# Kernel optimization log

Hardware: AMD Instinct MI355X
Metric: run time of the kernel (lower is better)

## Reference

```python
import jax, jax.numpy as jnp
import numpy as np

S, B, D, H, F = 2048, 4, 1024, 2, 2048
HD = D // H  # head dim = 512
EPS = 1e-8   # forward() hardcodes 1e-8, ignoring init eps


def rmsnorm(x, w):
    ms = jnp.mean(x * x, axis=-1, keepdims=True)
    return w * (x / jnp.sqrt(ms + EPS))


def setup_inputs() -> dict:
    key = jax.random.key(0)
    ks = jax.random.split(key, 12)
    s = 0.02
    return {
        "x": jax.random.normal(ks[0], (S, B, D), jnp.float32),
        "w_norm1": 1.0 + s * jax.random.normal(ks[1], (D,), jnp.float32),
        "in_proj_w": s * jax.random.normal(ks[2], (3 * D, D), jnp.float32),
        "in_proj_b": s * jax.random.normal(ks[3], (3 * D,), jnp.float32),
        "out_proj_w": s * jax.random.normal(ks[4], (D, D), jnp.float32),
        "out_proj_b": s * jax.random.normal(ks[5], (D,), jnp.float32),
        "w_norm2": 1.0 + s * jax.random.normal(ks[6], (D,), jnp.float32),
        "W1": s * jax.random.normal(ks[7], (F, D), jnp.float32),
        "b1": s * jax.random.normal(ks[8], (F,), jnp.float32),
        "W2": s * jax.random.normal(ks[9], (D, F), jnp.float32),
        "b2": s * jax.random.normal(ks[10], (D,), jnp.float32),
    }


def reference(x, w_norm1, in_proj_w, in_proj_b, out_proj_w, out_proj_b,
              w_norm2, W1, b1, W2, b2):
    # pre-norm
    h = rmsnorm(x, w_norm1)                      # (S,B,D)
    # packed qkv projection (torch MultiheadAttention in_proj)
    qkv = h @ in_proj_w.T + in_proj_b            # (S,B,3D)
    q, k, v = jnp.split(qkv, 3, axis=-1)
    # (S,B,D) -> (B,H,S,HD)
    def heads(t):
        return t.reshape(S, B, H, HD).transpose(1, 2, 0, 3)
    q, k, v = heads(q), heads(k), heads(v)
    scores = jnp.einsum("bhsd,bhtd->bhst", q, k) / jnp.sqrt(jnp.float32(HD))
    causal = jnp.tril(jnp.ones((S, S), bool))
    scores = jnp.where(causal, scores, -jnp.inf)
    attn = jax.nn.softmax(scores, axis=-1)       # (B,H,S,S)
    ctx = jnp.einsum("bhst,bhtd->bhsd", attn, v)  # (B,H,S,HD)
    ctx = ctx.transpose(2, 0, 1, 3).reshape(S, B, D)
    attn_out = ctx @ out_proj_w.T + out_proj_b
    # residual 1
    x1 = x + attn_out
    # MLP: Linear -> exact GELU -> Linear
    m = rmsnorm(x1, w_norm2)
    mlp = jax.nn.gelu(m @ W1.T + b1, approximate=False) @ W2.T + b2
    return x1 + mlp
```

## Files before the change

kernel.cpp:

```cpp
#include <hip/hip_runtime.h>


typedef __bf16 bf16;
typedef bf16 bf16x8 __attribute__((ext_vector_type(8)));
typedef bf16 bf16x4 __attribute__((ext_vector_type(4)));
typedef float f32x4 __attribute__((ext_vector_type(4)));

#define MFMA16x16x32(A, B, C) __builtin_amdgcn_mfma_f32_16x16x32_bf16(A, B, C, 0, 0, 0)

__device__ __forceinline__ void gload16(const void* g, void* l) {
  __builtin_amdgcn_global_load_lds(
      (const __attribute__((address_space(1))) void*)g,
      (__attribute__((address_space(3))) void*)l, 16, 0, 0);
}

__global__ __launch_bounds__(256) void wcvt(
    const float* __restrict__ src, bf16* __restrict__ dst, int n)
{
  const int i = (blockIdx.x * 256 + threadIdx.x) * 4;
  if (i < n) {
    const float4 v = *(const float4*)(src + i);
    bf16x4 o;
    o[0] = (bf16)v.x; o[1] = (bf16)v.y; o[2] = (bf16)v.z; o[3] = (bf16)v.w;
    *(bf16x4*)(dst + i) = o;
  }
}

__global__ __launch_bounds__(256) void rmsnorm_kernel(
    const float* __restrict__ x, const float* __restrict__ w, bf16* __restrict__ out)
{
  const int row = blockIdx.x;
  const int tid = threadIdx.x;
  const float4 v = *(const float4*)(x + (size_t)row * 1024 + tid * 4);
  float ss = v.x * v.x + v.y * v.y + v.z * v.z + v.w * v.w;
#pragma unroll
  for (int off = 1; off < 64; off <<= 1) ss += __shfl_xor(ss, off, 64);
  __shared__ float red[4];
  if ((tid & 63) == 0) red[tid >> 6] = ss;
  __syncthreads();
  const float tot = red[0] + red[1] + red[2] + red[3];
  const float inv = rsqrtf(tot * (1.0f / 1024.0f) + 1e-8f);
  const float4 g = *(const float4*)(w + tid * 4);
  bf16x4 o;
  o[0] = (bf16)(v.x * g.x * inv);
  o[1] = (bf16)(v.y * g.y * inv);
  o[2] = (bf16)(v.z * g.z * inv);
  o[3] = (bf16)(v.w * g.w * inv);
  *(bf16x4*)(out + (size_t)row * 1024 + tid * 4) = o;
}

enum { EPI_BF16 = 0, EPI_RES = 1, EPI_GELU = 2, EPI_QKV = 3 };

template <int EPI>
__global__ __launch_bounds__(256, 3) void gemm_bt2(
    const bf16* __restrict__ A,
    const bf16* __restrict__ B,
    const float* __restrict__ bias,
    const float* res,
    float* outF, bf16* outQ, bf16* outK, bf16* outV,
    int M, int N, int K)
{
  __shared__ bf16 As[128 * 32];
  __shared__ bf16 Bs[128 * 32];
  const int tid = threadIdx.x;
  const int Nb = N >> 7;
  const int lin = blockIdx.x;
  const int sup = lin / (Nb << 4);
  const int rem = lin - sup * (Nb << 4);
  const int bm = (sup << 4) + (rem & 15);
  const int bn = rem >> 4;
  const int w = tid >> 6, lane = tid & 63;
  const int q = lane >> 4, lr = lane & 15;
  const int wr = (w >> 1) * 64, wc = (w & 1) * 64;
  f32x4 acc[4][4] = {};
  const int srow = lane >> 2;
  const int gch = ((lane & 3) - ((lane >> 3) & 3)) & 3;
  const bf16* Ab = A + (size_t)(bm * 128) * K;
  const bf16* Bb = B + (size_t)(bn * 128) * K;
  const int sw = ((q + (lr >> 1)) & 3) * 16;

  for (int k0 = 0; k0 < K; k0 += 32) {
    __syncthreads();
#pragma unroll
    for (int c = 0; c < 2; c++) {
      const int r = (w * 2 + c) * 16 + srow;
      gload16(Ab + (size_t)r * K + k0 + gch * 8, &As[(w * 2 + c) * 512]);
      gload16(Bb + (size_t)r * K + k0 + gch * 8, &Bs[(w * 2 + c) * 512]);
    }
    __syncthreads();
    bf16x8 af[4], bfr[4];
#pragma unroll
    for (int mt = 0; mt < 4; mt++)
      af[mt] = *(const bf16x8*)((const char*)As + (wr + mt * 16 + lr) * 64 + sw);
#pragma unroll
    for (int nt = 0; nt < 4; nt++)
      bfr[nt] = *(const bf16x8*)((const char*)Bs + (wc + nt * 16 + lr) * 64 + sw);
#pragma unroll
    for (int mt = 0; mt < 4; mt++)
#pragma unroll
      for (int nt = 0; nt < 4; nt++)
        acc[mt][nt] = MFMA16x16x32(af[mt], bfr[nt], acc[mt][nt]);
  }
  const int gm0 = bm * 128 + wr + q * 4;
  const int gn0 = bn * 128 + wc + lr;
  bf16* outs = nullptr;
  if constexpr (EPI == EPI_QKV) {
    const int reg = (bn * 128) >> 10;
    outs = reg == 0 ? outQ : (reg == 1 ? outK : outV);
  } else {
    outs = outQ;
  }
#pragma unroll
  for (int nt = 0; nt < 4; nt++) {
    const int gn = gn0 + nt * 16;
    const float bv = bias[gn];
#pragma unroll
    for (int mt = 0; mt < 4; mt++) {
#pragma unroll
      for (int r = 0; r < 4; r++) {
        float v = acc[mt][nt][r] + bv;
        const int gm = gm0 + mt * 16 + r;
        if constexpr (EPI == EPI_GELU) {
          v = 0.5f * v * (1.0f + erff(v * 0.70710678118654752f));
          outs[(size_t)gm * N + gn] = (bf16)v;
        } else if constexpr (EPI == EPI_BF16) {
          outs[(size_t)gm * N + gn] = (bf16)v;
        } else if constexpr (EPI == EPI_QKV) {
          outs[(size_t)gm * 1024 + (gn & 1023)] = (bf16)v;
        } else {
          const size_t idx = (size_t)gm * N + gn;
          outF[idx] = v + res[idx];
        }
      }
    }
  }
}

__global__ __launch_bounds__(256) void vtrans_kernel(
    const bf16* __restrict__ vtmp, bf16* __restrict__ vt)
{
  __shared__ bf16 tile[64 * 72];
  const int kt = blockIdx.x;
  const int dt = blockIdx.y;
  const int bh = blockIdx.z;
  const int b = bh >> 1, h = bh & 1;
  const int tid = threadIdx.x;
#pragma unroll
  for (int it = 0; it < 2; it++) {
    const int key = it * 32 + (tid >> 3);
    const int dc = (tid & 7) * 8;
    const bf16x8 v = *(const bf16x8*)(vtmp +
        (size_t)((kt * 64 + key) * 4 + b) * 1024 + h * 512 + dt * 64 + dc);
    *(bf16x8*)&tile[key * 72 + dc] = v;
  }
  __syncthreads();
#pragma unroll
  for (int it = 0; it < 2; it++) {
    const int dim = it * 32 + (tid >> 3);
    const int kc = (tid & 7) * 8;
    bf16x8 o;
#pragma unroll
    for (int j = 0; j < 8; j++) o[j] = tile[(kc + j) * 72 + dim];
    *(bf16x8*)(vt + (size_t)bh * (1u << 20) +
               (size_t)(dt * 64 + dim) * 2048 + kt * 64 + kc) = o;
  }
}

__global__ __launch_bounds__(768, 3) void attn_kernel(
    const bf16* __restrict__ qb, const bf16* __restrict__ kb,
    const bf16* __restrict__ vtg, bf16* __restrict__ opart,
    float* __restrict__ lpart)
{
  __shared__ bf16 Ks[2][32 * 520];
  __shared__ bf16 Ps[2][4][16 * 40];
  const int bh = blockIdx.x;
  const int y = blockIdx.y;
  const int b = bh >> 1, h = bh & 1;
  const int tid = threadIdx.x;
  const int w = tid >> 6, lane = tid & 63;
  const int q = lane >> 4, lr = lane & 15;
  const float sc = 0.044194173824159216f;

  if (w < 4) {
    const bf16* krow0 = kb + (size_t)b * 1024 + h * 512 + lane * 8;
    for (int piece = 0; piece < 2; ++piece) {
      const int qt = piece ? (31 - y) : y;
      const int qrow0 = qt * 64;
      const int c0 = piece ? (qt + 1) : 0;
      const int c1 = c0 + qt + 1;
      bf16x8 Qf[16];
      {
        const bf16* qp = qb + (size_t)((qrow0 + w * 16 + lr) * 4 + b) * 1024 + h * 512 + q * 8;
#pragma unroll
        for (int kk = 0; kk < 16; kk++) Qf[kk] = *(const bf16x8*)(qp + kk * 32);
      }
#pragma unroll
      for (int j = 0; j < 8; j++)
        gload16(krow0 + (size_t)((c0 * 32 + w * 8 + j) * 4) * 1024,
                &Ks[c0 & 1][(w * 8 + j) * 520]);
      __syncthreads();
      const int myrow = qrow0 + w * 16 + q * 4;
      for (int t = c0; t <= c1; t++) {
        if (t < c1) {
          const int p = t & 1;
          const int kc = t * 32;
          if (t + 1 < c1) {
            const int kc2 = (t + 1) * 32;
#pragma unroll
            for (int j = 0; j < 8; j++)
              gload16(krow0 + (size_t)((kc2 + w * 8 + j) * 4) * 1024,
                      &Ks[1 - p][(w * 8 + j) * 520]);
          }
          const bool dead = kc > qrow0 + w * 16 + 15;
          float p0[4], p1[4];
          if (!dead) {
            f32x4 S0 = {}, S1 = {};
#pragma unroll
            for (int kk = 0; kk < 16; kk++) {
              const bf16x8 k0 = *(const bf16x8*)&Ks[p][lr * 520 + kk * 32 + q * 8];
              const bf16x8 k1 = *(const bf16x8*)&Ks[p][(16 + lr) * 520 + kk * 32 + q * 8];
              S0 = MFMA16x16x32(Qf[kk], k0, S0);
              S1 = MFMA16x16x32(Qf[kk], k1, S1);
            }
#pragma unroll
            for (int r = 0; r < 4; r++) {
              const int row = myrow + r;
              p0[r] = (kc + lr > row) ? 0.f : __expf(S0[r] * sc);
              p1[r] = (kc + 16 + lr > row) ? 0.f : __expf(S1[r] * sc);
            }
          } else {
#pragma unroll
            for (int r = 0; r < 4; r++) { p0[r] = 0.f; p1[r] = 0.f; }
          }
#pragma unroll
          for (int r = 0; r < 4; r++) {
            Ps[p][w][(q * 4 + r) * 40 + lr] = (bf16)p0[r];
            Ps[p][w][(q * 4 + r) * 40 + 16 + lr] = (bf16)p1[r];
          }
        }
        __syncthreads();
      }
    }
  } else {
    const int pw = w - 4;
    bf16x8 ones;
#pragma unroll
    for (int e = 0; e < 8; e++) ones[e] = (bf16)1.0f;
    const bf16* vbase = vtg + ((size_t)bh << 20) + (size_t)(pw * 64 + lr) * 2048 + q * 8;
    for (int piece = 0; piece < 2; ++piece) {
      const int qt = piece ? (31 - y) : y;
      const int qrow0 = qt * 64;
      const int c0 = piece ? (qt + 1) : 0;
      const int c1 = c0 + qt + 1;
      f32x4 O[4][4] = {};
      f32x4 lac = {};
      __syncthreads();
      for (int t = c0; t <= c1; t++) {
        if (t > c0) {
          const int p = (t - 1) & 1;
          const int kc = (t - 1) * 32;
          bf16x8 pa[4];
#pragma unroll
          for (int rt = 0; rt < 4; rt++)
            pa[rt] = *(const bf16x8*)&Ps[p][rt][lr * 40 + q * 8];
          if (pw < 4) {
            const bf16x8 psel = pw == 0 ? pa[0] : (pw == 1 ? pa[1] : (pw == 2 ? pa[2] : pa[3]));
            lac = MFMA16x16x32(psel, ones, lac);
          }
#pragma unroll
          for (int ct = 0; ct < 4; ct++) {
            const bf16x8 vf = *(const bf16x8*)(vbase + (size_t)(ct * 16) * 2048 + kc);
#pragma unroll
            for (int rt = 0; rt < 4; rt++)
              O[rt][ct] = MFMA16x16x32(pa[rt], vf, O[rt][ct]);
          }
        }
        __syncthreads();
      }
      bf16* op = opart + (size_t)piece * (8u << 20) + (size_t)bh * (1u << 20);
#pragma unroll
      for (int rt = 0; rt < 4; rt++)
#pragma unroll
        for (int ct = 0; ct < 4; ct++)
#pragma unroll
          for (int r = 0; r < 4; r++)
            op[(size_t)(qrow0 + rt * 16 + q * 4 + r) * 512 + pw * 64 + ct * 16 + lr] =
                (bf16)O[rt][ct][r];
      if (lr == 0 && pw < 4) {
#pragma unroll
        for (int r = 0; r < 4; r++)
          lpart[piece * 16384 + bh * 2048 + qrow0 + pw * 16 + q * 4 + r] = lac[r];
      }
    }
  }
}

__global__ __launch_bounds__(256) void attn_combine(
    const bf16* __restrict__ opart, const float* __restrict__ lpart,
    bf16* __restrict__ ctx)
{
  const int gid = blockIdx.x * 256 + threadIdx.x;
  const int bh = gid >> 17;
  const int rem = gid & 131071;
  const int row = rem >> 6;
  const int dc = (rem & 63) * 8;
  const size_t o = (size_t)bh * (1u << 20) + (size_t)row * 512 + dc;
  const bf16x8 a = *(const bf16x8*)(opart + o);
  const bf16x8 c = *(const bf16x8*)(opart + (size_t)(8u << 20) + o);
  const float inv = 1.0f /
      (lpart[bh * 2048 + row] + lpart[16384 + bh * 2048 + row]);
  bf16x8 ov;
#pragma unroll
  for (int e = 0; e < 8; e++) ov[e] = (bf16)(((float)a[e] + (float)c[e]) * inv);
  const int b = bh >> 1, h = bh & 1;
  *(bf16x8*)(ctx + (size_t)(row * 4 + b) * 1024 + h * 512 + dc) = ov;
}

extern "C" void kernel_launch(void* const* d_in, const int* in_sizes, int n_in,
                              void* d_out, int out_size, void* d_ws, size_t ws_size,
                              hipStream_t stream)
{
  (void)in_sizes; (void)n_in; (void)out_size; (void)ws_size;
  const float* x    = (const float*)d_in[0];
  const float* wn1  = (const float*)d_in[1];
  const float* wqkv = (const float*)d_in[2];
  const float* bqkv = (const float*)d_in[3];
  const float* wout = (const float*)d_in[4];
  const float* bout = (const float*)d_in[5];
  const float* wn2  = (const float*)d_in[6];
  const float* W1   = (const float*)d_in[7];
  const float* b1   = (const float*)d_in[8];
  const float* W2   = (const float*)d_in[9];
  const float* b2   = (const float*)d_in[10];
  float* out = (float*)d_out;

  char* ws = (char*)d_ws;
  const size_t Mi = 1u << 20;
  bf16* S0v = (bf16*)(ws);
  bf16* S1v = (bf16*)(ws + 16 * Mi);
  bf16* S2v = (bf16*)(ws + 32 * Mi);
  bf16* S3v = (bf16*)(ws + 48 * Mi);
  bf16* wqb = (bf16*)(ws + 64 * Mi);
  bf16* wob = (bf16*)(ws + 70 * Mi);
  bf16* w1b = (bf16*)(ws + 72 * Mi);
  bf16* w2b = (bf16*)(ws + 76 * Mi);
  const int M = 8192;

  wcvt<<<3072, 256, 0, stream>>>(wqkv, wqb, 3145728);
  wcvt<<<1024, 256, 0, stream>>>(wout, wob, 1048576);
  wcvt<<<2048, 256, 0, stream>>>(W1, w1b, 2097152);
  wcvt<<<2048, 256, 0, stream>>>(W2, w2b, 2097152);
  rmsnorm_kernel<<<8192, 256, 0, stream>>>(x, wn1, S0v);
  gemm_bt2<EPI_QKV><<<64 * 24, 256, 0, stream>>>(
      S0v, wqb, bqkv, nullptr, nullptr, S1v, S2v, S3v, M, 3072, 1024);
  vtrans_kernel<<<dim3(32, 8, 8), 256, 0, stream>>>(S3v, S0v);
  attn_kernel<<<dim3(8, 32), 768, 0, stream>>>(
      S1v, S2v, S0v, (bf16*)d_out, (float*)S3v);
  attn_combine<<<4096, 256, 0, stream>>>((const bf16*)d_out, (const float*)S3v, S1v);
  gemm_bt2<EPI_RES><<<64 * 8, 256, 0, stream>>>(
      S1v, wob, bout, x, out, nullptr, nullptr, nullptr, M, 1024, 1024);
  rmsnorm_kernel<<<8192, 256, 0, stream>>>(out, wn2, S0v);
  gemm_bt2<EPI_GELU><<<64 * 16, 256, 0, stream>>>(
      S0v, w1b, b1, nullptr, nullptr, S2v, nullptr, nullptr, M, 2048, 1024);
  gemm_bt2<EPI_RES><<<64 * 8, 256, 0, stream>>>(
      S2v, w2b, b2, out, out, nullptr, nullptr, nullptr, M, 1024, 2048);
}
```

Measured before the change: 424.6 us.

## Add 256x256-tile triple-buffered GEMM for QKV and MLP up-projection

Introduces a new GEMM kernel with 256x256 output tiles, 512 threads, three-stage LDS buffering via direct global-to-LDS loads, a swizzled LDS layout, XCD-aware block remapping and raised wave priority around the MFMA section. It replaces the older gemm_bt2 for the QKV projection and the GELU up-projection. Larger tiles are meant to raise arithmetic intensity and cut global traffic per FLOP. In exchange there are far fewer blocks (384 and 256), which may underfill the 256 CUs, and each thread holds 128 accumulator floats, which raises register pressure.

```diff
diff --git a/kernel.cpp b/kernel.cpp
--- a/kernel.cpp
+++ b/kernel.cpp
@@ -136,6 +136,113 @@
   }
 }
 
+template <int EPI>
+__global__ __launch_bounds__(512, 2) void gemm256(
+    const bf16* __restrict__ A,
+    const bf16* __restrict__ B,
+    const float* __restrict__ bias,
+    bf16* __restrict__ outQ, bf16* __restrict__ outK, bf16* __restrict__ outV,
+    int M, int N, int K)
+{
+  __shared__ bf16 lds[49152];
+  const int tid = threadIdx.x;
+  const int w = tid >> 6, lane = tid & 63;
+  const int q = lane >> 4, lr = lane & 15;
+  const int wm = w >> 2, wn = w & 3;
+  const int nbn = N >> 8;
+  const int cpx = gridDim.x >> 3;
+  const int lin = blockIdx.x;
+  const int wg = (lin & 7) * cpx + (lin >> 3);
+  const int bm = wg / nbn, bn = wg - bm * nbn;
+  const bf16* Ab = A + (size_t)(bm * 256) * K;
+  const bf16* Bb = B + (size_t)(bn * 256) * K;
+  const int srow = lane >> 2;
+  const int gch = ((lane & 3) - ((lane >> 3) & 3)) & 3;
+  const int sw = ((q + (lr >> 1)) & 3) * 16;
+  f32x4 acc[8][4] = {};
+  const int NK = K >> 5;
+
+#define STAGE256(dst, k0)                                                   \
+  {                                                                         \
+    bf16* De = (dst);                                                       \
+    _Pragma("unroll")                                                       \
+    for (int c = 0; c < 2; c++) {                                           \
+      const int r = w * 32 + c * 16 + srow;                                 \
+      gload16(Ab + (size_t)r * K + (k0) + gch * 8, De + (w * 32 + c * 16) * 32); \
+      gload16(Bb + (size_t)r * K + (k0) + gch * 8, De + 8192 + (w * 32 + c * 16) * 32); \
+    }                                                                       \
+  }
+
+  STAGE256(&lds[0], 0);
+  STAGE256(&lds[16384], 32);
+  asm volatile("s_waitcnt vmcnt(4)" ::: "memory");
+  __builtin_amdgcn_s_barrier();
+  asm volatile("" ::: "memory");
+
+  bf16* rd = &lds[0];
+  bf16* nx = &lds[16384];
+  bf16* st = &lds[32768];
+#pragma unroll 1
+  for (int u = 0; u < NK; ++u) {
+    if (u + 2 < NK) STAGE256(st, (u + 2) * 32);
+    const char* As = (const char*)rd;
+    const char* Bs = (const char*)(rd + 8192);
+    bf16x8 af[8], bfr[4];
+    __builtin_amdgcn_s_setprio(1);
+#pragma unroll
+    for (int mt = 0; mt < 8; mt++)
+      af[mt] = *(const bf16x8*)(As + (wm * 128 + mt * 16 + lr) * 64 + sw);
+#pragma unroll
+    for (int nt = 0; nt < 4; nt++)
+      bfr[nt] = *(const bf16x8*)(Bs + (wn * 64 + nt * 16 + lr) * 64 + sw);
+#pragma unroll
+    for (int mt = 0; mt < 8; mt++)
+#pragma unroll
+      for (int nt = 0; nt < 4; nt++)
+        acc[mt][nt] = MFMA16x16x32(af[mt], bfr[nt], acc[mt][nt]);
+    __builtin_amdgcn_s_setprio(0);
+    if (u + 1 < NK) {
+      if (u + 2 < NK)
+        asm volatile("s_waitcnt vmcnt(4) lgkmcnt(0)" ::: "memory");
+      else
+        asm volatile("s_waitcnt vmcnt(0) lgkmcnt(0)" ::: "memory");
+      __builtin_amdgcn_s_barrier();
+      asm volatile("" ::: "memory");
+    }
+    bf16* t = rd; rd = nx; nx = st; st = t;
+  }
+#undef STAGE256
+
+  const int gm0 = bm * 256 + wm * 128 + q * 4;
+  const int gn0 = bn * 256 + wn * 64 + lr;
+  bf16* outs;
+  if constexpr (EPI == EPI_QKV) {
+    const int reg = bn >> 2;
+    outs = reg == 0 ? outQ : (reg == 1 ? outK : outV);
+  } else {
+    outs = outQ;
+  }
+#pragma unroll
+  for (int nt = 0; nt < 4; nt++) {
+    const int gn = gn0 + nt * 16;
+    const float bv = bias[gn];
+#pragma unroll
+    for (int mt = 0; mt < 8; mt++) {
+#pragma unroll
+      for (int r = 0; r < 4; r++) {
+        float v = acc[mt][nt][r] + bv;
+        const int gm = gm0 + mt * 16 + r;
+        if constexpr (EPI == EPI_GELU) {
+          v = 0.5f * v * (1.0f + erff(v * 0.70710678118654752f));
+          outs[(size_t)gm * N + gn] = (bf16)v;
+        } else {
+          outs[(size_t)gm * 1024 + (gn & 1023)] = (bf16)v;
+        }
+      }
+    }
+  }
+}
+
 __global__ __launch_bounds__(256) void vtrans_kernel(
     const bf16* __restrict__ vtmp, bf16* __restrict__ vt)
 {
@@ -351,8 +458,8 @@
   wcvt<<<2048, 256, 0, stream>>>(W1, w1b, 2097152);
   wcvt<<<2048, 256, 0, stream>>>(W2, w2b, 2097152);
   rmsnorm_kernel<<<8192, 256, 0, stream>>>(x, wn1, S0v);
-  gemm_bt2<EPI_QKV><<<64 * 24, 256, 0, stream>>>(
-      S0v, wqb, bqkv, nullptr, nullptr, S1v, S2v, S3v, M, 3072, 1024);
+  gemm256<EPI_QKV><<<32 * 12, 512, 0, stream>>>(
+      S0v, wqb, bqkv, S1v, S2v, S3v, M, 3072, 1024);
   vtrans_kernel<<<dim3(32, 8, 8), 256, 0, stream>>>(S3v, S0v);
   attn_kernel<<<dim3(8, 32), 768, 0, stream>>>(
       S1v, S2v, S0v, (bf16*)d_out, (float*)S3v);
@@ -360,8 +467,8 @@
   gemm_bt2<EPI_RES><<<64 * 8, 256, 0, stream>>>(
       S1v, wob, bout, x, out, nullptr, nullptr, nullptr, M, 1024, 1024);
   rmsnorm_kernel<<<8192, 256, 0, stream>>>(out, wn2, S0v);
-  gemm_bt2<EPI_GELU><<<64 * 16, 256, 0, stream>>>(
-      S0v, w1b, b1, nullptr, nullptr, S2v, nullptr, nullptr, M, 2048, 1024);
+  gemm256<EPI_GELU><<<32 * 8, 512, 0, stream>>>(
+      S0v, w1b, b1, S2v, nullptr, nullptr, M, 2048, 1024);
   gemm_bt2<EPI_RES><<<64 * 8, 256, 0, stream>>>(
       S2v, w2b, b2, out, out, nullptr, nullptr, nullptr, M, 1024, 2048);
 }
```

Result: slower. 452.7 us (+6.6%).

## Triple-buffer GEMM LDS staging and merge weight conversion launches

Applied to the files above, without the earlier changes.

The GEMM main loop goes from a single LDS buffer with two barriers per k-step to a three-stage ring buffer. Global-to-LDS loads for step u+2 are issued before computing step u, with explicit vmcnt waits and one barrier per iteration. This is meant to hide global load latency behind MFMA work. LDS use per block grows from 16KB to 48KB, which may reduce occupancy under the 3-blocks launch bound. The four weight-conversion launches are also merged into one kernel to cut launch overhead.

```diff
diff --git a/kernel.cpp b/kernel.cpp
--- a/kernel.cpp
+++ b/kernel.cpp
@@ -14,16 +14,23 @@
       (__attribute__((address_space(3))) void*)l, 16, 0, 0);
 }
 
-__global__ __launch_bounds__(256) void wcvt(
-    const float* __restrict__ src, bf16* __restrict__ dst, int n)
-{
-  const int i = (blockIdx.x * 256 + threadIdx.x) * 4;
-  if (i < n) {
-    const float4 v = *(const float4*)(src + i);
-    bf16x4 o;
-    o[0] = (bf16)v.x; o[1] = (bf16)v.y; o[2] = (bf16)v.z; o[3] = (bf16)v.w;
-    *(bf16x4*)(dst + i) = o;
-  }
+__global__ __launch_bounds__(256) void wcvt4(
+    const float* __restrict__ s0, bf16* __restrict__ d0,
+    const float* __restrict__ s1, bf16* __restrict__ d1,
+    const float* __restrict__ s2, bf16* __restrict__ d2,
+    const float* __restrict__ s3, bf16* __restrict__ d3)
+{
+  const int gid = blockIdx.x * 256 + threadIdx.x;
+  const float* s; bf16* d; int off;
+  if (gid < 786432)       { s = s0; d = d0; off = gid; }
+  else if (gid < 1048576) { s = s1; d = d1; off = gid - 786432; }
+  else if (gid < 1572864) { s = s2; d = d2; off = gid - 1048576; }
+  else                    { s = s3; d = d3; off = gid - 1572864; }
+  const int i = off * 4;
+  const float4 v = *(const float4*)(s + i);
+  bf16x4 o;
+  o[0] = (bf16)v.x; o[1] = (bf16)v.y; o[2] = (bf16)v.z; o[3] = (bf16)v.w;
+  *(bf16x4*)(d + i) = o;
 }
 
 __global__ __launch_bounds__(256) void rmsnorm_kernel(
@@ -60,8 +67,7 @@
     float* outF, bf16* outQ, bf16* outK, bf16* outV,
     int M, int N, int K)
 {
-  __shared__ bf16 As[128 * 32];
-  __shared__ bf16 Bs[128 * 32];
+  __shared__ bf16 lds[3 * 8192];
   const int tid = threadIdx.x;
   const int Nb = N >> 7;
   const int lin = blockIdx.x;
@@ -78,29 +84,57 @@
   const bf16* Ab = A + (size_t)(bm * 128) * K;
   const bf16* Bb = B + (size_t)(bn * 128) * K;
   const int sw = ((q + (lr >> 1)) & 3) * 16;
-
-  for (int k0 = 0; k0 < K; k0 += 32) {
-    __syncthreads();
-#pragma unroll
-    for (int c = 0; c < 2; c++) {
-      const int r = (w * 2 + c) * 16 + srow;
-      gload16(Ab + (size_t)r * K + k0 + gch * 8, &As[(w * 2 + c) * 512]);
-      gload16(Bb + (size_t)r * K + k0 + gch * 8, &Bs[(w * 2 + c) * 512]);
-    }
-    __syncthreads();
+  const int NK = K >> 5;
+
+#define STAGE(dst, k0)                                                        \
+  {                                                                           \
+    bf16* De = (dst);                                                         \
+    _Pragma("unroll")                                                         \
+    for (int c = 0; c < 2; c++) {                                             \
+      const int r = (w * 2 + c) * 16 + srow;                                  \
+      gload16(Ab + (size_t)r * K + (k0) + gch * 8, De + (w * 2 + c) * 512);   \
+      gload16(Bb + (size_t)r * K + (k0) + gch * 8, De + 4096 + (w * 2 + c) * 512); \
+    }                                                                         \
+  }
+
+  bf16* rd = &lds[0];
+  bf16* nx = &lds[8192];
+  bf16* st = &lds[16384];
+  STAGE(rd, 0);
+  STAGE(nx, 32);
+  asm volatile("s_waitcnt vmcnt(2)" ::: "memory");
+  __builtin_amdgcn_s_barrier();
+  asm volatile("" ::: "memory");
+
+#pragma unroll 1
+  for (int u = 0; u < NK; ++u) {
+    if (u + 2 < NK) STAGE(st, (u + 2) * 32);
+    const char* As = (const char*)rd;
+    const char* Bs = (const char*)(rd + 4096);
     bf16x8 af[4], bfr[4];
 #pragma unroll
     for (int mt = 0; mt < 4; mt++)
-      af[mt] = *(const bf16x8*)((const char*)As + (wr + mt * 16 + lr) * 64 + sw);
+      af[mt] = *(const bf16x8*)(As + (wr + mt * 16 + lr) * 64 + sw);
 #pragma unroll
     for (int nt = 0; nt < 4; nt++)
-      bfr[nt] = *(const bf16x8*)((const char*)Bs + (wc + nt * 16 + lr) * 64 + sw);
+      bfr[nt] = *(const bf16x8*)(Bs + (wc + nt * 16 + lr) * 64 + sw);
 #pragma unroll
     for (int mt = 0; mt < 4; mt++)
 #pragma unroll
       for (int nt = 0; nt < 4; nt++)
         acc[mt][nt] = MFMA16x16x32(af[mt], bfr[nt], acc[mt][nt]);
-  }
+    if (u + 1 < NK) {
+      if (u + 2 < NK)
+        asm volatile("s_waitcnt vmcnt(2) lgkmcnt(0)" ::: "memory");
+      else
+        asm volatile("s_waitcnt vmcnt(0) lgkmcnt(0)" ::: "memory");
+      __builtin_amdgcn_s_barrier();
+      asm volatile("" ::: "memory");
+    }
+    bf16* t = rd; rd = nx; nx = st; st = t;
+  }
+#undef STAGE
+
   const int gm0 = bm * 128 + wr + q * 4;
   const int gn0 = bn * 128 + wc + lr;
   bf16* outs = nullptr;
@@ -346,10 +380,7 @@
   bf16* w2b = (bf16*)(ws + 76 * Mi);
   const int M = 8192;
 
-  wcvt<<<3072, 256, 0, stream>>>(wqkv, wqb, 3145728);
-  wcvt<<<1024, 256, 0, stream>>>(wout, wob, 1048576);
-  wcvt<<<2048, 256, 0, stream>>>(W1, w1b, 2097152);
-  wcvt<<<2048, 256, 0, stream>>>(W2, w2b, 2097152);
+  wcvt4<<<8192, 256, 0, stream>>>(wqkv, wqb, wout, wob, W1, w1b, W2, w2b);
   rmsnorm_kernel<<<8192, 256, 0, stream>>>(x, wn1, S0v);
   gemm_bt2<EPI_QKV><<<64 * 24, 256, 0, stream>>>(
       S0v, wqb, bqkv, nullptr, nullptr, S1v, S2v, S3v, M, 3072, 1024);
```

Result: no change. 420.4 us (-1.0%).
